# Kernel optimization log

Hardware: AMD Instinct MI355X
Metric: run time of the kernel (lower is better)

The kernel has to match this reference:

```python
import jax, jax.numpy as jnp
import numpy as np

D_MODEL = 1024
N_HEADS = 16
BATCH = 2
SEQ = 2048


def get_freqs(seq, n_dim):
    # standard RoPE frequencies: [seq, n_dim//2]
    inv_freq = 1.0 / (10000.0 ** (jnp.arange(0, n_dim, 2, dtype=jnp.float32) / n_dim))
    return jnp.arange(seq, dtype=jnp.float32)[:, None] * inv_freq[None, :]


def rope(x, freqs):
    # x: [batch, seq, heads, n_dim]; half-split rotation convention
    half = x.shape[-1] // 2
    cos = jnp.cos(freqs)[None, :, None, :]  # [1, seq, 1, half]
    sin = jnp.sin(freqs)[None, :, None, :]
    x1, x2 = x[..., :half], x[..., half:]
    return jnp.concatenate([x1 * cos - x2 * sin, x1 * sin + x2 * cos], axis=-1)


def setup_inputs() -> dict:
    key = jax.random.key(0)
    ks = jax.random.split(key, 5)
    x = jax.random.normal(ks[0], (BATCH, SEQ, D_MODEL), dtype=jnp.float32)
    qw = jax.random.normal(ks[1], (D_MODEL, D_MODEL), dtype=jnp.float32)
    kw = jax.random.normal(ks[2], (D_MODEL, D_MODEL), dtype=jnp.float32)
    vw = jax.random.normal(ks[3], (D_MODEL, D_MODEL), dtype=jnp.float32)
    ow = jax.random.normal(ks[4], (D_MODEL, D_MODEL), dtype=jnp.float32)
    return {"x": x, "qw": qw, "kw": kw, "vw": vw, "ow": ow}


def reference(x, qw, kw, vw, ow):
    batch, seq, dim = x.shape
    n_heads = N_HEADS
    n_dim = dim // n_heads
    Q = (x @ qw).reshape(batch, seq, n_heads, n_dim)
    K = (x @ kw).reshape(batch, seq, n_heads, n_dim)
    V = (x @ vw).reshape(batch, seq, n_heads, n_dim)
    freqs = get_freqs(seq, n_dim)
    Q = rope(Q, freqs)
    K = rope(K, freqs)
    # NOTE: original divides by sqrt(d_model), not sqrt(head_dim)
    scale = 1.0 / jnp.sqrt(jnp.float32(dim))
    score = jnp.einsum('bqhd,bkhd->bhqk', Q, K) * scale
    weights = jax.nn.softmax(score.astype(jnp.float32), axis=-1)
    attn = jnp.einsum('bhqk,bkhd->bqhd', weights, V)
    merged = attn.reshape(batch, seq, dim)
    return merged @ ow
```

## Files before the change

kernel.cpp:

```cpp
#include <hip/hip_runtime.h>
#include <math.h>

#define DM 1024
#define NH 16
#define HD 64
#define BB 2
#define SS 2048
#define MM (BB*SS)

typedef unsigned short ushort_t;
typedef __attribute__((ext_vector_type(8))) short short8;
typedef __attribute__((ext_vector_type(4))) short short4_t;
typedef __attribute__((ext_vector_type(4))) float floatx4;

__device__ __forceinline__ ushort_t f2bf(float f) {
    return (ushort_t)((__float_as_uint(f) + 0x8000u) >> 16);
}
__device__ __forceinline__ float bf2f(ushort_t h) {
    return __uint_as_float(((unsigned int)h) << 16);
}

__device__ __forceinline__ void gl_lds16(const ushort_t* g, ushort_t* l) {
    __builtin_amdgcn_global_load_lds(
        (const __attribute__((address_space(1))) unsigned int*)g,
        (__attribute__((address_space(3))) unsigned int*)l, 16, 0, 0);
}

__global__ __launch_bounds__(256) void freq_kernel(float2* __restrict__ ct)
{
    const int idx = blockIdx.x * 256 + threadIdx.x;
    const int s = idx >> 5, j = idx & 31;
    const float invf = powf(10000.f, -(float)j * (1.f / 32.f));
    float sn, cs;
    sincosf((float)s * invf, &sn, &cs);
    ct[idx] = make_float2(cs, sn);
}

__global__ __launch_bounds__(256) void convert_x(const float* __restrict__ X,
                                                 ushort_t* __restrict__ Xh,
                                                 ushort_t* __restrict__ Xl)
{
    const size_t base = ((size_t)blockIdx.x * 256 + threadIdx.x) * 8;
    float v[8];
    *(float4*)&v[0] = *(const float4*)(X + base);
    *(float4*)&v[4] = *(const float4*)(X + base + 4);
    short8 h, l;
#pragma unroll
    for (int i = 0; i < 8; ++i) {
        const ushort_t hi = f2bf(v[i]);
        h[i] = (short)hi;
        l[i] = (short)f2bf(v[i] - bf2f(hi));
    }
    *(short8*)(Xh + base) = h;
    *(short8*)(Xl + base) = l;
}

__global__ __launch_bounds__(256) void convert_w4(
    const float* __restrict__ qw, const float* __restrict__ kw,
    const float* __restrict__ vw, const float* __restrict__ ow,
    ushort_t* __restrict__ qkh, ushort_t* __restrict__ qkl,
    ushort_t* __restrict__ vwt, ushort_t* __restrict__ owt)
{
    const int which = blockIdx.z;
    const float* W;
    ushort_t *Th, *Tl = nullptr;
    bool split = which < 2;
    if (which == 0)      { W = qw; Th = qkh; Tl = qkl; }
    else if (which == 1) { W = kw; Th = qkh + (size_t)DM * DM; Tl = qkl + (size_t)DM * DM; }
    else if (which == 2) { W = vw; Th = vwt; }
    else                 { W = ow; Th = owt; }

    __shared__ float tile[64][65];
    const int t  = threadIdx.x;
    const int kb = blockIdx.y * 64, nb = blockIdx.x * 64;
    const int r  = t >> 2;
    const int c0 = (t & 3) * 16;
#pragma unroll
    for (int i = 0; i < 4; ++i)
        *(float4*)&tile[r][c0 + 4 * i] = *(const float4*)(W + (size_t)(kb + r) * DM + nb + c0 + 4 * i);
    __syncthreads();
    ushort_t hi[16], lo[16];
#pragma unroll
    for (int i = 0; i < 16; ++i) {
        const float v = tile[c0 + i][r];
        hi[i] = f2bf(v);
        lo[i] = f2bf(v - bf2f(hi[i]));
    }
    const size_t dst = (size_t)(nb + r) * DM + kb + c0;
    *(short8*)(Th + dst)     = *(short8*)&hi[0];
    *(short8*)(Th + dst + 8) = *(short8*)&hi[8];
    if (split) {
        *(short8*)(Tl + dst)     = *(short8*)&lo[0];
        *(short8*)(Tl + dst + 8) = *(short8*)&lo[8];
    }
}

#define GTM 128

template<int UPR, int SH>
__device__ __forceinline__ void stage_tile(const ushort_t* __restrict__ G,
                                           ushort_t* L, int rows, int w, int lane)
{
    const int iters = rows * UPR / 256;
#pragma unroll
    for (int i = 0; i < iters; ++i) {
        const int p0 = (i * 4 + w) * 64;
        const int p  = p0 + lane;
        const int r  = p / UPR;
        const int u  = (p % UPR) ^ ((r >> SH) & (UPR - 1));
        gl_lds16(G + (size_t)r * DM + u * 8, L + (size_t)p0 * 8);
    }
}

template<int UPR, int SH>
__device__ __forceinline__ short8 frag(const ushort_t* L, int r, int u)
{
    const int uu = u ^ ((r >> SH) & (UPR - 1));
    return *(const short8*)&L[((size_t)r * UPR + uu) * 8];
}

template<int SPLIT, int OUT_MODE, int TN, int BK>
__global__ __launch_bounds__(256, 2) void gemm_mfma(
    const ushort_t* __restrict__ Ah, const ushort_t* __restrict__ Al,
    const ushort_t* __restrict__ Bh, const ushort_t* __restrict__ Bl,
    float* __restrict__ Cf, ushort_t* __restrict__ Cb, ushort_t* __restrict__ Cb2,
    const float2* __restrict__ CT)
{
    constexpr int UPR = BK / 8;
    constexpr int KC  = BK / 32;
    constexpr int NI  = TN / 32;
    constexpr int SH  = (UPR == 4) ? 1 : 0;
    constexpr int NSTEP = DM / BK;

    __shared__ __align__(16) ushort_t AsH[2][GTM * BK];
    __shared__ __align__(16) ushort_t BsH[2][TN * BK];
    __shared__ __align__(16) ushort_t AsL[2][SPLIT ? GTM * BK : 8];
    __shared__ __align__(16) ushort_t BsL[2][SPLIT ? TN * BK : 8];
    __shared__ __align__(16) ushort_t Ts[(OUT_MODE == 2) ? 64 * 136 : 8];

    const int t    = threadIdx.x;
    const int w    = t >> 6;
    const int lane = t & 63;
    const int col  = lane & 15;
    const int quad = lane >> 4;
    const int wm   = w & 1;
    const int wn   = w >> 1;
    const int m0   = blockIdx.y * GTM;
    const int n0   = blockIdx.x * TN;

    const ushort_t* Abase = Ah + (size_t)m0 * DM;
    const ushort_t* Bbase = Bh + (size_t)n0 * DM;
    const ushort_t* AbaseL = SPLIT ? Al + (size_t)m0 * DM : nullptr;
    const ushort_t* BbaseL = SPLIT ? Bl + (size_t)n0 * DM : nullptr;

    floatx4 acc[4][NI];
#pragma unroll
    for (int mi = 0; mi < 4; ++mi)
#pragma unroll
        for (int ni = 0; ni < NI; ++ni) acc[mi][ni] = (floatx4){0.f, 0.f, 0.f, 0.f};

    stage_tile<UPR, SH>(Abase, AsH[0], GTM, w, lane);
    if (SPLIT) stage_tile<UPR, SH>(AbaseL, AsL[0], GTM, w, lane);
    stage_tile<UPR, SH>(Bbase, BsH[0], TN, w, lane);
    if (SPLIT) stage_tile<UPR, SH>(BbaseL, BsL[0], TN, w, lane);

    for (int ks = 0; ks < NSTEP; ++ks) {
        const int cur = ks & 1;
        __syncthreads();
        if (ks + 1 < NSTEP) {
            const int k1 = (ks + 1) * BK;
            stage_tile<UPR, SH>(Abase + k1, AsH[cur ^ 1], GTM, w, lane);
            if (SPLIT) stage_tile<UPR, SH>(AbaseL + k1, AsL[cur ^ 1], GTM, w, lane);
            stage_tile<UPR, SH>(Bbase + k1, BsH[cur ^ 1], TN, w, lane);
            if (SPLIT) stage_tile<UPR, SH>(BbaseL + k1, BsL[cur ^ 1], TN, w, lane);
        }

#pragma unroll
        for (int kc = 0; kc < KC; ++kc) {
            short8 ah[4], bh[NI];
            short8 al[SPLIT ? 4 : 1], bl[SPLIT ? NI : 1];
#pragma unroll
            for (int mi = 0; mi < 4; ++mi) {
                const int r = wm * 64 + mi * 16 + col;
                ah[mi] = frag<UPR, SH>(AsH[cur], r, kc * 4 + quad);
                if (SPLIT) al[mi] = frag<UPR, SH>(AsL[cur], r, kc * 4 + quad);
            }
#pragma unroll
            for (int ni = 0; ni < NI; ++ni) {
                const int r = wn * (TN / 2) + ni * 16 + col;
                bh[ni] = frag<UPR, SH>(BsH[cur], r, kc * 4 + quad);
                if (SPLIT) bl[ni] = frag<UPR, SH>(BsL[cur], r, kc * 4 + quad);
            }
#pragma unroll
            for (int mi = 0; mi < 4; ++mi)
#pragma unroll
                for (int ni = 0; ni < NI; ++ni) {
                    acc[mi][ni] = __builtin_amdgcn_mfma_f32_16x16x32_bf16(ah[mi], bh[ni], acc[mi][ni], 0, 0, 0);
                    if (SPLIT) {
                        acc[mi][ni] = __builtin_amdgcn_mfma_f32_16x16x32_bf16(al[mi], bh[ni], acc[mi][ni], 0, 0, 0);
                        acc[mi][ni] = __builtin_amdgcn_mfma_f32_16x16x32_bf16(ah[mi], bl[ni], acc[mi][ni], 0, 0, 0);
                    }
                }
        }
    }

    if constexpr (OUT_MODE == 0) {
#pragma unroll
        for (int mi = 0; mi < 4; ++mi)
#pragma unroll
            for (int ni = 0; ni < NI; ++ni)
#pragma unroll
                for (int r = 0; r < 4; ++r) {
                    const int m = m0 + wm * 64 + mi * 16 + quad * 4 + r;
                    const int n = n0 + wn * (TN / 2) + ni * 16 + col;
                    Cf[(size_t)m * DM + n] = acc[mi][ni][r];
                }
    }
    if constexpr (OUT_MODE == 2) {
#pragma unroll
        for (int mi = 0; mi < 4; ++mi)
#pragma unroll
            for (int ni = 0; ni < NI; ++ni) {
                const int nl = wn * (TN / 2) + ni * 16 + col;
                const int ml = wm * 64 + mi * 16 + quad * 4;
                short4_t pk;
#pragma unroll
                for (int r = 0; r < 4; ++r) pk[r] = (short)f2bf(acc[mi][ni][r]);
                *(short4_t*)&Ts[nl * 136 + ml] = pk;
            }
        __syncthreads();
        const int b = m0 >> 11, h = n0 >> 6;
        const int s0 = m0 & (SS - 1);
#pragma unroll
        for (int it = 0; it < 4; ++it) {
            const int idx = it * 256 + t;
            const int dr = idx >> 4, u = idx & 15;
            const short8 v = *(const short8*)&Ts[dr * 136 + u * 8];
            *(short8*)(Cb + ((size_t)((b << 4) + h) * HD + dr) * SS + s0 + u * 8) = v;
        }
    }
    if constexpr (OUT_MODE == 3) {
        const int tn = n0 >> 10;
#pragma unroll
        for (int mi = 0; mi < 4; ++mi)
#pragma unroll
            for (int ni = 0; ni < 2; ++ni)
#pragma unroll
                for (int r = 0; r < 4; ++r) {
                    const int m = m0 + wm * 64 + mi * 16 + quad * 4 + r;
                    const int n = n0 + wn * (TN / 2) + ni * 16 + col;
                    const int b = m >> 11, s = m & (SS - 1);
                    const int h = (n >> 6) & 15, d = n & 63;
                    const float2 cs = CT[(s << 5) + d];
                    const float x1 = acc[mi][ni][r];
                    const float x2 = acc[mi][ni + 2][r];
                    const float y1 = x1 * cs.x - x2 * cs.y;
                    const float y2 = x1 * cs.y + x2 * cs.x;
                    const size_t base = ((size_t)((b << 4) + h) * SS + s) * HD + d;
                    if (tn == 0) {
                        Cf[base]      = y1 * (1.f / 32.f);
                        Cf[base + 32] = y2 * (1.f / 32.f);
                    } else {
                        const ushort_t h1 = f2bf(y1), h2 = f2bf(y2);
                        Cb [base]      = h1;
                        Cb [base + 32] = h2;
                        Cb2[base]      = f2bf(y1 - bf2f(h1));
                        Cb2[base + 32] = f2bf(y2 - bf2f(h2));
                    }
                }
    }
}

__device__ __forceinline__ short8 afrag(const ushort_t* S, int r, int lu)
{
    return *(const short8*)&S[(size_t)(((r << 3) | (lu ^ (r & 7))) << 3)];
}

__global__ __launch_bounds__(256, 2) void attn_split(
    const float* __restrict__ Qh, const ushort_t* __restrict__ Khi,
    const ushort_t* __restrict__ Klo, const ushort_t* __restrict__ Vt,
    ushort_t* __restrict__ Op0, ushort_t* __restrict__ Op1,
    float2* __restrict__ ML)
{
    __shared__ __align__(16) ushort_t KhiS[64 * 64];
    __shared__ __align__(16) ushort_t KloS[64 * 64];
    __shared__ __align__(16) ushort_t VtS [64 * 64];
    __shared__ __align__(16) ushort_t PS  [128 * 64];

    const int t    = threadIdx.x;
    const int w    = t >> 6;
    const int lane = t & 63;
    const int col  = lane & 15;
    const int quad = lane >> 4;

    const int bh   = blockIdx.y;
    const int q0   = blockIdx.x * 128;
    const int z    = blockIdx.z;
    const int koff = z * (SS / 2);
    const float*    Qb  = Qh  + (size_t)bh * SS * HD;
    const ushort_t* KhB = Khi + (size_t)bh * SS * HD;
    const ushort_t* KlB = Klo + (size_t)bh * SS * HD;
    const ushort_t* VtB = Vt  + (size_t)bh * HD * SS;

    short8 qhi[2][2], qlo[2][2];
#pragma unroll
    for (int mi = 0; mi < 2; ++mi) {
#pragma unroll
        for (int ch = 0; ch < 2; ++ch) {
            const float* p = Qb + (size_t)(q0 + w * 32 + mi * 16 + col) * HD + ch * 32 + quad * 8;
            const float4 a = *(const float4*)p;
            const float4 b = *(const float4*)(p + 4);
            float v[8] = {a.x, a.y, a.z, a.w, b.x, b.y, b.z, b.w};
#pragma unroll
            for (int j = 0; j < 8; ++j) {
                const ushort_t h = f2bf(v[j]);
                qhi[mi][ch][j] = (short)h;
                qlo[mi][ch][j] = (short)f2bf(v[j] - bf2f(h));
            }
        }
    }

    floatx4 Oacc[2][4];
#pragma unroll
    for (int mi = 0; mi < 2; ++mi)
#pragma unroll
        for (int nt = 0; nt < 4; ++nt) Oacc[mi][nt] = (floatx4){0.f, 0.f, 0.f, 0.f};
    float mstat[2] = {-1e30f, -1e30f}, lstat[2] = {0.f, 0.f};

    for (int kt0 = 0; kt0 < (SS / 2) / 64; ++kt0) {
        const int k0 = koff + kt0 * 64;
        __syncthreads();
#pragma unroll
        for (int i = 0; i < 2; ++i) {
            const int p0 = w * 128 + i * 64;
            const int p  = p0 + lane;
            const int r  = p >> 3;
            const int gu = (p & 7) ^ (r & 7);
            gl_lds16(KhB + (size_t)(k0 + r) * HD + gu * 8, KhiS + (size_t)p0 * 8);
            gl_lds16(KlB + (size_t)(k0 + r) * HD + gu * 8, KloS + (size_t)p0 * 8);
            gl_lds16(VtB + (size_t)r * SS + k0 + gu * 8,   VtS  + (size_t)p0 * 8);
        }
        __syncthreads();

        floatx4 sc[4][2];
#pragma unroll
        for (int kt = 0; kt < 4; ++kt) {
            short8 kh[2], kl[2];
#pragma unroll
            for (int ch = 0; ch < 2; ++ch) {
                kh[ch] = afrag(KhiS, kt * 16 + col, ch * 4 + quad);
                kl[ch] = afrag(KloS, kt * 16 + col, ch * 4 + quad);
            }
#pragma unroll
            for (int mi = 0; mi < 2; ++mi) {
                floatx4 a = (floatx4){0.f, 0.f, 0.f, 0.f};
#pragma unroll
                for (int ch = 0; ch < 2; ++ch)
                    a = __builtin_amdgcn_mfma_f32_16x16x32_bf16(kh[ch], qhi[mi][ch], a, 0, 0, 0);
#pragma unroll
                for (int ch = 0; ch < 2; ++ch)
                    a = __builtin_amdgcn_mfma_f32_16x16x32_bf16(kh[ch], qlo[mi][ch], a, 0, 0, 0);
#pragma unroll
                for (int ch = 0; ch < 2; ++ch)
                    a = __builtin_amdgcn_mfma_f32_16x16x32_bf16(kl[ch], qhi[mi][ch], a, 0, 0, 0);
                sc[kt][mi] = a;
            }
        }

#pragma unroll
        for (int mi = 0; mi < 2; ++mi) {
            float mloc = -1e30f;
#pragma unroll
            for (int kt = 0; kt < 4; ++kt)
#pragma unroll
                for (int r = 0; r < 4; ++r) mloc = fmaxf(mloc, sc[kt][mi][r]);
            mloc = fmaxf(mloc, __shfl_xor(mloc, 16));
            mloc = fmaxf(mloc, __shfl_xor(mloc, 32));
            const float mnew  = fmaxf(mstat[mi], mloc);
            const float alpha = __expf(mstat[mi] - mnew);
            mstat[mi] = mnew;

            float psum = 0.f;
            const int qrow = w * 32 + mi * 16 + col;
#pragma unroll
            for (int kt = 0; kt < 4; ++kt) {
                short4_t pk;
#pragma unroll
                for (int r = 0; r < 4; ++r) {
                    const float p = __expf(sc[kt][mi][r] - mnew);
                    psum += p;
                    pk[r] = (short)f2bf(p);
                }
                const int u = (kt * 2 + (quad >> 1)) ^ (col & 7);
                *(short4_t*)&PS[(qrow << 6) + (u << 3) + ((quad & 1) << 2)] = pk;
            }
            psum += __shfl_xor(psum, 16);
            psum += __shfl_xor(psum, 32);
            lstat[mi] = lstat[mi] * alpha + psum;

            floatx4 alr;
#pragma unroll
            for (int r = 0; r < 4; ++r) alr[r] = __shfl(alpha, quad * 4 + r, 64);
#pragma unroll
            for (int nt = 0; nt < 4; ++nt)
#pragma unroll
                for (int r = 0; r < 4; ++r) Oacc[mi][nt][r] *= alr[r];
        }

        short8 pf[2][2];
#pragma unroll
        for (int mi = 0; mi < 2; ++mi)
#pragma unroll
            for (int ch = 0; ch < 2; ++ch)
                pf[mi][ch] = afrag(PS, w * 32 + mi * 16 + col, ch * 4 + quad);
#pragma unroll
        for (int nt = 0; nt < 4; ++nt) {
            short8 vf[2];
#pragma unroll
            for (int ch = 0; ch < 2; ++ch)
                vf[ch] = afrag(VtS, nt * 16 + col, ch * 4 + quad);
#pragma unroll
            for (int mi = 0; mi < 2; ++mi)
#pragma unroll
                for (int ch = 0; ch < 2; ++ch)
                    Oacc[mi][nt] = __builtin_amdgcn_mfma_f32_16x16x32_bf16(pf[mi][ch], vf[ch], Oacc[mi][nt], 0, 0, 0);
        }
    }

    ushort_t* dst = z ? Op1 : Op0;
    const int b = bh >> 4, h = bh & 15;
#pragma unroll
    for (int mi = 0; mi < 2; ++mi) {
#pragma unroll
        for (int nt = 0; nt < 4; ++nt)
#pragma unroll
            for (int r = 0; r < 4; ++r) {
                const int srow = q0 + w * 32 + mi * 16 + quad * 4 + r;
                dst[(size_t)(b * SS + srow) * DM + h * HD + nt * 16 + col] =
                    f2bf(Oacc[mi][nt][r]);
            }
        if (quad == 0) {
            const int srow = q0 + w * 32 + mi * 16 + col;
            ML[((size_t)z * 32 + bh) * SS + srow] = make_float2(mstat[mi], lstat[mi]);
        }
    }
}

__global__ __launch_bounds__(256) void attn_combine(
    ushort_t* __restrict__ Op0, const ushort_t* __restrict__ Op1,
    const float2* __restrict__ ML)
{
    const size_t idx8 = ((size_t)blockIdx.x * 256 + threadIdx.x) * 8;
    const int row  = (int)(idx8 >> 10);
    const int hcol = (int)(idx8 & 1023);
    const int h = hcol >> 6;
    const int b = row >> 11, s = row & (SS - 1);
    const int bh = (b << 4) + h;

    const float2 ml0 = ML[(size_t)bh * SS + s];
    const float2 ml1 = ML[((size_t)32 + bh) * SS + s];
    const float m  = fmaxf(ml0.x, ml1.x);
    const float s0 = __expf(ml0.x - m);
    const float s1 = __expf(ml1.x - m);
    const float inv = 1.f / (s0 * ml0.y + s1 * ml1.y);

    const short8 a = *(const short8*)(Op0 + idx8);
    const short8 c = *(const short8*)(Op1 + idx8);
    short8 o;
#pragma unroll
    for (int i = 0; i < 8; ++i)
        o[i] = (short)f2bf((s0 * bf2f((ushort_t)a[i]) + s1 * bf2f((ushort_t)c[i])) * inv);
    *(short8*)(Op0 + idx8) = o;
}

extern "C" void kernel_launch(void* const* d_in, const int* in_sizes, int n_in,
                              void* d_out, int out_size, void* d_ws, size_t ws_size,
                              hipStream_t stream)
{
    const float* x  = (const float*)d_in[0];
    const float* qw = (const float*)d_in[1];
    const float* kw = (const float*)d_in[2];
    const float* vw = (const float*)d_in[3];
    const float* ow = (const float*)d_in[4];
    float* out = (float*)d_out;

    float*    Qh  = (float*)d_ws;
    ushort_t* Khi = (ushort_t*)(Qh + (size_t)MM * DM);
    ushort_t* Klo = Khi + (size_t)MM * DM;
    ushort_t* Vtb = Klo + (size_t)MM * DM;
    ushort_t* Mgb = Vtb + (size_t)MM * DM;
    ushort_t* xh  = Mgb + (size_t)MM * DM;
    ushort_t* xl  = xh  + (size_t)MM * DM;
    ushort_t* qkh = xl  + (size_t)MM * DM;
    ushort_t* qkl = qkh + (size_t)2048 * DM;
    ushort_t* vwt = qkl + (size_t)2048 * DM;
    ushort_t* owt = vwt + (size_t)DM * DM;
    float2*   ct  = (float2*)(owt + (size_t)DM * DM);

    ushort_t* Op1 = xh;
    float2*   ML  = (float2*)xl;

    freq_kernel<<<(SS * 32) / 256, 256, 0, stream>>>(ct);
    convert_x<<<(MM * DM) / (256 * 8), 256, 0, stream>>>(x, xh, xl);
    convert_w4<<<dim3(16, 16, 4), 256, 0, stream>>>(qw, kw, vw, ow, qkh, qkl, vwt, owt);

    gemm_mfma<1, 3, 128, 32><<<dim3(2048 / 128, MM / GTM), 256, 0, stream>>>(
        xh, xl, qkh, qkl, Qh, Khi, Klo, ct);
    gemm_mfma<0, 2, 64, 64><<<dim3(DM / 64, MM / GTM), 256, 0, stream>>>(
        xh, nullptr, vwt, nullptr, nullptr, Vtb, nullptr, nullptr);

    attn_split<<<dim3(SS / 128, BB * NH, 2), 256, 0, stream>>>(
        Qh, Khi, Klo, Vtb, Mgb, Op1, ML);
    attn_combine<<<(MM * DM) / (256 * 8), 256, 0, stream>>>(Mgb, Op1, ML);

    gemm_mfma<0, 0, 64, 64><<<dim3(DM / 64, MM / GTM), 256, 0, stream>>>(
        Mgb, nullptr, owt, nullptr, out, nullptr, nullptr, nullptr);
}
```

Before: 279.0 us.

## Single-buffer GEMM LDS tiles and fold log2e into Q for exp2 softmax

The GEMM kernel drops its double-buffered LDS prefetch and instead stages each K tile into a single buffer between two barriers, halving shared memory use. The intent is likely to raise occupancy or cut register pressure, at the cost of no longer overlapping global loads with MFMA work. Separately, Q is pre-scaled by log2(e) in the projection epilogue so that softmax and combine can use the hardware exp2 instruction instead of __expf, removing a multiply per exponent.

```diff
diff --git a/kernel.cpp b/kernel.cpp
--- a/kernel.cpp
+++ b/kernel.cpp
@@ -130,12 +130,11 @@
     constexpr int KC  = BK / 32;
     constexpr int NI  = TN / 32;
     constexpr int SH  = (UPR == 4) ? 1 : 0;
-    constexpr int NSTEP = DM / BK;
-
-    __shared__ __align__(16) ushort_t AsH[2][GTM * BK];
-    __shared__ __align__(16) ushort_t BsH[2][TN * BK];
-    __shared__ __align__(16) ushort_t AsL[2][SPLIT ? GTM * BK : 8];
-    __shared__ __align__(16) ushort_t BsL[2][SPLIT ? TN * BK : 8];
+
+    __shared__ __align__(16) ushort_t AsH[GTM * BK];
+    __shared__ __align__(16) ushort_t BsH[TN * BK];
+    __shared__ __align__(16) ushort_t AsL[SPLIT ? GTM * BK : 8];
+    __shared__ __align__(16) ushort_t BsL[SPLIT ? TN * BK : 8];
     __shared__ __align__(16) ushort_t Ts[(OUT_MODE == 2) ? 64 * 136 : 8];
 
     const int t    = threadIdx.x;
@@ -148,32 +147,19 @@
     const int m0   = blockIdx.y * GTM;
     const int n0   = blockIdx.x * TN;
 
-    const ushort_t* Abase = Ah + (size_t)m0 * DM;
-    const ushort_t* Bbase = Bh + (size_t)n0 * DM;
-    const ushort_t* AbaseL = SPLIT ? Al + (size_t)m0 * DM : nullptr;
-    const ushort_t* BbaseL = SPLIT ? Bl + (size_t)n0 * DM : nullptr;
-
     floatx4 acc[4][NI];
 #pragma unroll
     for (int mi = 0; mi < 4; ++mi)
 #pragma unroll
         for (int ni = 0; ni < NI; ++ni) acc[mi][ni] = (floatx4){0.f, 0.f, 0.f, 0.f};
 
-    stage_tile<UPR, SH>(Abase, AsH[0], GTM, w, lane);
-    if (SPLIT) stage_tile<UPR, SH>(AbaseL, AsL[0], GTM, w, lane);
-    stage_tile<UPR, SH>(Bbase, BsH[0], TN, w, lane);
-    if (SPLIT) stage_tile<UPR, SH>(BbaseL, BsL[0], TN, w, lane);
-
-    for (int ks = 0; ks < NSTEP; ++ks) {
-        const int cur = ks & 1;
+    for (int k0 = 0; k0 < DM; k0 += BK) {
         __syncthreads();
-        if (ks + 1 < NSTEP) {
-            const int k1 = (ks + 1) * BK;
-            stage_tile<UPR, SH>(Abase + k1, AsH[cur ^ 1], GTM, w, lane);
-            if (SPLIT) stage_tile<UPR, SH>(AbaseL + k1, AsL[cur ^ 1], GTM, w, lane);
-            stage_tile<UPR, SH>(Bbase + k1, BsH[cur ^ 1], TN, w, lane);
-            if (SPLIT) stage_tile<UPR, SH>(BbaseL + k1, BsL[cur ^ 1], TN, w, lane);
-        }
+        stage_tile<UPR, SH>(Ah + (size_t)m0 * DM + k0, AsH, GTM, w, lane);
+        if (SPLIT) stage_tile<UPR, SH>(Al + (size_t)m0 * DM + k0, AsL, GTM, w, lane);
+        stage_tile<UPR, SH>(Bh + (size_t)n0 * DM + k0, BsH, TN, w, lane);
+        if (SPLIT) stage_tile<UPR, SH>(Bl + (size_t)n0 * DM + k0, BsL, TN, w, lane);
+        __syncthreads();
 
 #pragma unroll
         for (int kc = 0; kc < KC; ++kc) {
@@ -182,14 +168,14 @@
 #pragma unroll
             for (int mi = 0; mi < 4; ++mi) {
                 const int r = wm * 64 + mi * 16 + col;
-                ah[mi] = frag<UPR, SH>(AsH[cur], r, kc * 4 + quad);
-                if (SPLIT) al[mi] = frag<UPR, SH>(AsL[cur], r, kc * 4 + quad);
+                ah[mi] = frag<UPR, SH>(AsH, r, kc * 4 + quad);
+                if (SPLIT) al[mi] = frag<UPR, SH>(AsL, r, kc * 4 + quad);
             }
 #pragma unroll
             for (int ni = 0; ni < NI; ++ni) {
                 const int r = wn * (TN / 2) + ni * 16 + col;
-                bh[ni] = frag<UPR, SH>(BsH[cur], r, kc * 4 + quad);
-                if (SPLIT) bl[ni] = frag<UPR, SH>(BsL[cur], r, kc * 4 + quad);
+                bh[ni] = frag<UPR, SH>(BsH, r, kc * 4 + quad);
+                if (SPLIT) bl[ni] = frag<UPR, SH>(BsL, r, kc * 4 + quad);
             }
 #pragma unroll
             for (int mi = 0; mi < 4; ++mi)
@@ -258,8 +244,9 @@
                     const float y2 = x1 * cs.y + x2 * cs.x;
                     const size_t base = ((size_t)((b << 4) + h) * SS + s) * HD + d;
                     if (tn == 0) {
-                        Cf[base]      = y1 * (1.f / 32.f);
-                        Cf[base + 32] = y2 * (1.f / 32.f);
+                        const float qs = 1.442695041f / 32.f;
+                        Cf[base]      = y1 * qs;
+                        Cf[base + 32] = y2 * qs;
                     } else {
                         const ushort_t h1 = f2bf(y1), h2 = f2bf(y2);
                         Cb [base]      = h1;
@@ -377,7 +364,7 @@
             mloc = fmaxf(mloc, __shfl_xor(mloc, 16));
             mloc = fmaxf(mloc, __shfl_xor(mloc, 32));
             const float mnew  = fmaxf(mstat[mi], mloc);
-            const float alpha = __expf(mstat[mi] - mnew);
+            const float alpha = __builtin_amdgcn_exp2f(mstat[mi] - mnew);
             mstat[mi] = mnew;
 
             float psum = 0.f;
@@ -387,7 +374,7 @@
                 short4_t pk;
 #pragma unroll
                 for (int r = 0; r < 4; ++r) {
-                    const float p = __expf(sc[kt][mi][r] - mnew);
+                    const float p = __builtin_amdgcn_exp2f(sc[kt][mi][r] - mnew);
                     psum += p;
                     pk[r] = (short)f2bf(p);
                 }
@@ -460,8 +447,8 @@
     const float2 ml0 = ML[(size_t)bh * SS + s];
     const float2 ml1 = ML[((size_t)32 + bh) * SS + s];
     const float m  = fmaxf(ml0.x, ml1.x);
-    const float s0 = __expf(ml0.x - m);
-    const float s1 = __expf(ml1.x - m);
+    const float s0 = __builtin_amdgcn_exp2f(ml0.x - m);
+    const float s1 = __builtin_amdgcn_exp2f(ml1.x - m);
     const float inv = 1.f / (s0 * ml0.y + s1 * ml1.y);
 
     const short8 a = *(const short8*)(Op0 + idx8);
```

Result: faster. 262.7 us (median of 2 runs) (-5.9%).
